# Optimization experiments

Hardware: AMD Instinct MI355X
Metric: run time of the kernel (lower is better)

## Reference

```python
import jax, jax.numpy as jnp
import numpy as np

N = 20000
NNBR = 64
MESH = (64, 64, 64)
ORDER = 4          # B-spline interpolation order
ALPHA = 0.35       # Ewald splitting parameter (1/Angstrom)
BOX = 73.68        # cubic box edge (Angstrom)
KE = 14.399645478425668  # Coulomb constant, eV*Angstrom/e^2


def _Mn(x, n):
    """Cardinal B-spline M_n(x), support [0, n]."""
    if n == 2:
        return jnp.maximum(0.0, 1.0 - jnp.abs(x - 1.0))
    return (x * _Mn(x, n - 1) + (n - x) * _Mn(x - 1.0, n - 1)) / (n - 1)


def _bspline_fac(K):
    """|b(m)|^-2 ... i.e. 1/|Euler spline denominator|^2 per mesh dim."""
    m = jnp.arange(K, dtype=jnp.float32)
    k = jnp.arange(ORDER - 1, dtype=jnp.float32)
    Mv = _Mn(k + 1.0, ORDER)                       # M_n(1..n-1)
    phase = 2.0 * jnp.pi * m[:, None] * k[None, :] / K
    dre = jnp.sum(Mv * jnp.cos(phase), axis=1)
    dim = jnp.sum(Mv * jnp.sin(phase), axis=1)
    return 1.0 / (dre * dre + dim * dim)


def _pme_energy(positions, charges, cell, nbr, shifts):
    n = positions.shape[0]
    # ---------------- real-space short-range sum ----------------
    i_idx = jnp.arange(n)[:, None]
    valid = (nbr >= 0) & ~((nbr == i_idx) & jnp.all(shifts == 0, axis=-1))
    j = jnp.where(nbr >= 0, nbr, 0)
    rvec = positions[j] + shifts.astype(positions.dtype) @ cell - positions[:, None, :]
    r2 = jnp.sum(rvec * rvec, axis=-1)
    r = jnp.sqrt(jnp.where(valid, r2, 1.0))
    qq = charges[:, None] * charges[j]
    e_real = 0.5 * jnp.sum(jnp.where(valid, qq * jax.scipy.special.erfc(ALPHA * r) / r, 0.0))
    # ---------------- B-spline charge spreading ----------------
    Kx, Ky, Kz = MESH
    frac = positions @ jnp.linalg.inv(cell)        # cell rows = lattice vectors
    u = frac * jnp.array(MESH, dtype=positions.dtype)
    base = jnp.floor(u)
    t = u - base                                   # in [0, 1)
    basei = base.astype(jnp.int32)
    offs = jnp.arange(ORDER)
    wx = _Mn(t[:, 0:1] + offs, ORDER)              # [N, ORDER]
    wy = _Mn(t[:, 1:2] + offs, ORDER)
    wz = _Mn(t[:, 2:3] + offs, ORDER)
    ix = (basei[:, 0:1] - offs) % Kx
    iy = (basei[:, 1:2] - offs) % Ky
    iz = (basei[:, 2:3] - offs) % Kz
    W = (charges[:, None] * wx)[:, :, None, None] * wy[:, None, :, None] * wz[:, None, None, :]
    IDX = (ix[:, :, None, None] * Ky + iy[:, None, :, None]) * Kz + iz[:, None, None, :]
    mesh = jnp.zeros(Kx * Ky * Kz, positions.dtype).at[IDX.reshape(-1)].add(W.reshape(-1)).reshape(MESH)
    # ---------------- reciprocal-space FFT convolution ----------------
    Q = jnp.fft.fftn(mesh)
    Brec = 2.0 * jnp.pi * jnp.linalg.inv(cell).T   # rows are reciprocal vectors
    mx = (jnp.fft.fftfreq(Kx) * Kx).astype(positions.dtype)
    my = (jnp.fft.fftfreq(Ky) * Ky).astype(positions.dtype)
    mz = (jnp.fft.fftfreq(Kz) * Kz).astype(positions.dtype)
    kvec = (mx[:, None, None, None] * Brec[0] + my[None, :, None, None] * Brec[1]
            + mz[None, None, :, None] * Brec[2])
    k2 = jnp.sum(kvec * kvec, axis=-1)
    a2 = ALPHA * ALPHA
    kern = jnp.where(k2 > 0, jnp.exp(-k2 / (4.0 * a2)) / jnp.where(k2 > 0, k2, 1.0), 0.0)
    C = _bspline_fac(Kx)[:, None, None] * _bspline_fac(Ky)[None, :, None] * _bspline_fac(Kz)[None, None, :]
    vol = jnp.abs(jnp.linalg.det(cell))
    e_rec = (2.0 * jnp.pi / vol) * jnp.sum(kern * C * (Q.real ** 2 + Q.imag ** 2))
    # ---------------- self + neutralizing background ----------------
    qtot = jnp.sum(charges)
    e_self = -(ALPHA / jnp.sqrt(jnp.pi)) * jnp.sum(charges * charges)
    e_bg = -(jnp.pi / (2.0 * a2 * vol)) * qtot * qtot
    return e_real + e_rec + e_self + e_bg


def setup_inputs() -> dict:
    key = jax.random.key(0)
    k1, k2, k3 = jax.random.split(key, 3)
    positions = jax.random.uniform(k1, (N, 3), jnp.float32) * BOX
    q = jax.random.normal(k2, (N,), jnp.float32)
    q = q - jnp.mean(q)  # neutral system
    cell = BOX * jnp.eye(3, dtype=jnp.float32)
    nbr = jax.random.randint(k3, (N, NNBR), 0, N, jnp.int32)
    shifts = jnp.zeros((N, NNBR, 3), jnp.int32)
    return {"positions": positions, "node_charges": q, "cell": cell,
            "neighbor_matrix": nbr, "neighbor_shifts": shifts}


def reference(positions, node_charges, cell, neighbor_matrix, neighbor_shifts):
    def e_strain(pos, q, c, eps):
        F = jnp.eye(3, dtype=pos.dtype) + eps
        return _pme_energy(pos @ F, q, c @ F, neighbor_matrix, neighbor_shifts)

    eps0 = jnp.zeros((3, 3), positions.dtype)
    e, (g_pos, g_eps) = jax.value_and_grad(e_strain, argnums=(0, 3))(
        positions, node_charges, cell, eps0)
    vol = jnp.abs(jnp.linalg.det(cell))
    energies = e.reshape(1) * KE
    forces = -g_pos * KE
    virial = -0.5 * (g_eps + g_eps.T) * KE
    stresses = (virial / vol)[None]
    return energies, forces, stresses
```

## Files before the change

kernel.cpp:

```cpp
#include <hip/hip_runtime.h>
#include <math.h>

#define NATOM 20000
#define NNBR  64
#define KM    64
#define KM3   (KM*KM*KM)

#define ALPHA_C 0.35f
#define KE_C    14.399645478425668f
#define TWO_OVER_SQRTPI 1.1283791670955126f
#define TWOPI_F 6.2831853071795864f
#define PI_F    3.14159265358979f
#define RC2     661.2244898f

#define WS_RE    0
#define WS_IM    (KM3)
#define WS_MESH  (2*KM3)
#define WS_GJ    (3*KM3)
#define WS_PART  (3*KM3 + 3*NATOM)
#define WS_FI    (WS_PART + 1024)
#define WS_POSQ  (WS_FI + 3*NATOM)
#define ZERO_LEN (KM3 + 3*NATOM + 1024)

__device__ __forceinline__ float M2f(float x){ return fmaxf(0.f, 1.f - fabsf(x - 1.f)); }
__device__ __forceinline__ float M3f(float x){ return (x*M2f(x) + (3.f-x)*M2f(x-1.f)) * 0.5f; }
__device__ __forceinline__ float M4f(float x){ return (x*M3f(x) + (4.f-x)*M3f(x-1.f)) * (1.f/3.f); }

__device__ __forceinline__ float wsum64(float v){
#pragma unroll
  for(int off=32; off>0; off>>=1) v += __shfl_xor(v, off, 64);
  return v;
}

__device__ __forceinline__ float hinv9(const float* __restrict__ cell, float* h){
  float m00=cell[0],m01=cell[1],m02=cell[2];
  float m10=cell[3],m11=cell[4],m12=cell[5];
  float m20=cell[6],m21=cell[7],m22=cell[8];
  float det = m00*(m11*m22-m12*m21) - m01*(m10*m22-m12*m20) + m02*(m10*m21-m11*m20);
  float id = 1.f/det;
  h[0]=(m11*m22-m12*m21)*id; h[1]=(m02*m21-m01*m22)*id; h[2]=(m01*m12-m02*m11)*id;
  h[3]=(m12*m20-m10*m22)*id; h[4]=(m00*m22-m02*m20)*id; h[5]=(m02*m10-m00*m12)*id;
  h[6]=(m10*m21-m11*m20)*id; h[7]=(m01*m20-m00*m21)*id; h[8]=(m00*m11-m01*m10)*id;
  return fabsf(det);
}

__device__ __forceinline__ void fft64(float& xr, float& xi, int lane, float sgn8){
#pragma unroll
  for(int k=0;k<6;k++){
    int half = 32 >> k;
    float or_ = __shfl_xor(xr, half, 64);
    float oi_ = __shfl_xor(xi, half, 64);
    bool hi = (lane & half) != 0;
    float sr = hi ? (or_ - xr) : (xr + or_);
    float si = hi ? (oi_ - xi) : (xi + oi_);
    int e = (lane & (half-1)) << k;
    float ws, wc; sincosf(sgn8 * (float)e, &ws, &wc);
    float wr2 = hi ? wc : 1.f;
    float wi2 = hi ? ws : 0.f;
    xr = sr*wr2 - si*wi2;
    xi = sr*wi2 + si*wr2;
  }
  int rev = __brev((unsigned)lane) >> 26;
  xr = __shfl(xr, rev, 64);
  xi = __shfl(xi, rev, 64);
}

__global__ __launch_bounds__(256) void init_kernel(
    const float* __restrict__ pos, const float* __restrict__ q,
    float* __restrict__ zbase, float4* __restrict__ posq){
  int t = blockIdx.x*256 + threadIdx.x;
  if(t < ZERO_LEN) zbase[t] = 0.f;
  if(t < NATOM)
    posq[t] = make_float4(pos[3*t], pos[3*t+1], pos[3*t+2], q[t]);
}

__global__ __launch_bounds__(256) void real_kernel(
    const float4* __restrict__ posq,
    const int* __restrict__ nbr, const int* __restrict__ shifts,
    const float* __restrict__ cell,
    float* __restrict__ fi, float* __restrict__ gj, float* __restrict__ part){
  int lane = threadIdx.x & 63;
  int wid  = blockIdx.x*4 + (threadIdx.x>>6);
  float c0=cell[0],c1=cell[1],c2=cell[2];
  float c3=cell[3],c4=cell[4],c5=cell[5];
  float c6=cell[6],c7=cell[7],c8=cell[8];
  float e=0.f, vxx=0.f,vyy=0.f,vzz=0.f,vxy=0.f,vxz=0.f,vyz=0.f;
#pragma unroll
  for(int it=0; it<4; ++it){
    int i = wid*4 + it;
    float4 pi4 = posq[i];
    int p = i*NNBR + lane;
    int j = nbr[p];
    int sx=shifts[3*p], sy=shifts[3*p+1], sz=shifts[3*p+2];
    bool self = (j==i) && (sx==0) && (sy==0) && (sz==0);
    float s=0.f, rx=0.f, ry=0.f, rz=0.f;
    if(j>=0 && !self){
      float4 pj = posq[j];
      rx = pj.x - pi4.x + sx*c0 + sy*c3 + sz*c6;
      ry = pj.y - pi4.y + sx*c1 + sy*c4 + sz*c7;
      rz = pj.z - pi4.z + sx*c2 + sy*c5 + sz*c8;
      float r2 = rx*rx + ry*ry + rz*rz;
      if(r2 > 0.f && r2 < RC2){
        float r = sqrtf(r2);
        float ar = ALPHA_C * r;
        float qq = pi4.w * pj.w;
        float ef = erfcf(ar);
        float ex = expf(-ar*ar);
        float ir = 1.f/r;
        e += 0.5f*qq*ef*ir;
        s  = 0.5f*qq*(ef + TWO_OVER_SQRTPI*ar*ex)*ir*ir*ir;
      }
    }
    float gx = s*rx, gy = s*ry, gz = s*rz;
    if(s != 0.f){
      unsafeAtomicAdd(&gj[3*j+0], -gx);
      unsafeAtomicAdd(&gj[3*j+1], -gy);
      unsafeAtomicAdd(&gj[3*j+2], -gz);
    }
    vxx -= s*rx*rx; vyy -= s*ry*ry; vzz -= s*rz*rz;
    vxy -= s*rx*ry; vxz -= s*rx*rz; vyz -= s*ry*rz;
    float tgx = wsum64(gx), tgy = wsum64(gy), tgz = wsum64(gz);
    if(lane==0){ fi[3*i]=tgx; fi[3*i+1]=tgy; fi[3*i+2]=tgz; }
  }
  e   = wsum64(e);
  vxx = wsum64(vxx); vyy = wsum64(vyy); vzz = wsum64(vzz);
  vxy = wsum64(vxy); vxz = wsum64(vxz); vyz = wsum64(vyz);
  if(lane==0){
    float* slot = part + (wid & 63)*16;
    unsafeAtomicAdd(&slot[0], e);
    unsafeAtomicAdd(&slot[1], vxx); unsafeAtomicAdd(&slot[2], vyy); unsafeAtomicAdd(&slot[3], vzz);
    unsafeAtomicAdd(&slot[4], vxy); unsafeAtomicAdd(&slot[5], vxz); unsafeAtomicAdd(&slot[6], vyz);
  }
}

__global__ __launch_bounds__(256) void spread_kernel(
    const float4* __restrict__ posq, const float* __restrict__ cell,
    float* __restrict__ mesh){
  int wid  = blockIdx.x*4 + (threadIdx.x>>6);
  int lane = threadIdx.x & 63;
  float h[9]; hinv9(cell, h);
  float4 pq = posq[wid];
  float u0=(pq.x*h[0]+pq.y*h[3]+pq.z*h[6])*(float)KM;
  float u1=(pq.x*h[1]+pq.y*h[4]+pq.z*h[7])*(float)KM;
  float u2=(pq.x*h[2]+pq.y*h[5]+pq.z*h[8])*(float)KM;
  float b0=floorf(u0), b1=floorf(u1), b2=floorf(u2);
  float t0=u0-b0, t1=u1-b1, t2=u2-b2;
  int i0=(int)b0, i1=(int)b1, i2=(int)b2;
  int a = lane>>4, b = (lane>>2)&3, c = lane&3;
  float w = pq.w * M4f(t0+(float)a) * M4f(t1+(float)b) * M4f(t2+(float)c);
  int ix=(i0-a+256)&63, iy=(i1-b+256)&63, iz=(i2-c+256)&63;
  unsafeAtomicAdd(&mesh[(ix*KM + iy)*KM + iz], w);
}

__global__ __launch_bounds__(256) void fftA(const float* __restrict__ mesh,
                                            float* __restrict__ re, float* __restrict__ im){
  __shared__ float lr[64][65], li[64][65];
  int t = threadIdx.x, lane = t&63, w = t>>6;
  int x = blockIdx.x;
  const float sgn8 = -(TWOPI_F/64.f);
  const float* mp = mesh + x*4096;
#pragma unroll
  for(int qq=0; qq<16; qq++){
    int y = w*16 + qq;
    float xr = mp[y*64 + lane], xi = 0.f;
    fft64(xr, xi, lane, sgn8);
    lr[y][lane]=xr; li[y][lane]=xi;
  }
  __syncthreads();
#pragma unroll
  for(int qq=0; qq<16; qq++){
    int z = w*16 + qq;
    float xr = lr[lane][z], xi = li[lane][z];
    fft64(xr, xi, lane, sgn8);
    lr[lane][z]=xr; li[lane][z]=xi;
  }
  __syncthreads();
  float* rp = re + x*4096; float* ip = im + x*4096;
#pragma unroll
  for(int k=0;k<16;k++){
    int e = k*256 + t;
    rp[e]=lr[e>>6][e&63]; ip[e]=li[e>>6][e&63];
  }
}

__global__ __launch_bounds__(256) void fftB(float* __restrict__ re, float* __restrict__ im,
                                            const float* __restrict__ cell,
                                            float* __restrict__ part){
  __shared__ float lr[64][17], li[64][17], cf[64];
  int t = threadIdx.x, lane = t&63, w = t>>6;
  int y = blockIdx.x>>2, z0 = (blockIdx.x&3)*16;
  const float sgn8 = -(TWOPI_F/64.f);
  float h[9]; hinv9(cell, h);
  if(t < 64){
    float p1 = TWOPI_F*(float)t/64.f;
    float s1,c1_,s2,c2_; sincosf(p1,&s1,&c1_); sincosf(2.f*p1,&s2,&c2_);
    float dre = (1.f/6.f) + (2.f/3.f)*c1_ + (1.f/6.f)*c2_;
    float dim = (2.f/3.f)*s1 + (1.f/6.f)*s2;
    cf[t] = 1.f/(dre*dre + dim*dim);
  }
  float* rp = re + y*64 + z0;
  float* ip = im + y*64 + z0;
#pragma unroll
  for(int k=0;k<4;k++){
    int e = k*256 + t; int xI = e>>4, zz = e&15;
    lr[xI][zz] = rp[xI*4096 + zz];
    li[xI][zz] = ip[xI*4096 + zz];
  }
  __syncthreads();
  const float inv4a2 = 1.f/(4.f*ALPHA_C*ALPHA_C);
  float my_f = (float)((y<32)? y : y-64);
  float sE=0.f, v0=0.f,v1=0.f,v2=0.f,v3=0.f,v4=0.f,v5=0.f;
#pragma unroll
  for(int qq=0; qq<4; qq++){
    int zz = w*4 + qq; int z = z0 + zz;
    float xr = lr[lane][zz], xi = li[lane][zz];
    fft64(xr, xi, lane, sgn8);
    int mx = lane, mz = z;
    float fx = (float)((mx<32)? mx : mx-64);
    float fz = (float)((mz<32)? mz : mz-64);
    float kx = TWOPI_F*(fx*h[0] + my_f*h[1] + fz*h[2]);
    float ky = TWOPI_F*(fx*h[3] + my_f*h[4] + fz*h[5]);
    float kz = TWOPI_F*(fx*h[6] + my_f*h[7] + fz*h[8]);
    float k2 = kx*kx + ky*ky + kz*kz;
    float wk = 0.f;
    if(k2 > 0.f){
      float kern = expf(-k2*inv4a2)/k2;
      wk = kern * cf[mx]*cf[y]*cf[z];
      float q2 = xr*xr + xi*xi;
      sE += wk*q2;
      float fac = wk*q2*(inv4a2 + 1.f/k2)*2.f;
      v0 += fac*kx*kx; v1 += fac*ky*ky; v2 += fac*kz*kz;
      v3 += fac*kx*ky; v4 += fac*kx*kz; v5 += fac*ky*kz;
    }
    lr[lane][zz] = wk*xr; li[lane][zz] = wk*xi;
  }
  __syncthreads();
#pragma unroll
  for(int k=0;k<4;k++){
    int e = k*256 + t; int xI = e>>4, zz = e&15;
    rp[xI*4096 + zz] = lr[xI][zz];
    ip[xI*4096 + zz] = li[xI][zz];
  }
  sE = wsum64(sE);
  v0 = wsum64(v0); v1 = wsum64(v1); v2 = wsum64(v2);
  v3 = wsum64(v3); v4 = wsum64(v4); v5 = wsum64(v5);
  if(lane==0){
    float* slot = part + (((blockIdx.x<<2)|w)&63)*16;
    unsafeAtomicAdd(&slot[7],  sE);
    unsafeAtomicAdd(&slot[8],  v0); unsafeAtomicAdd(&slot[9],  v1);
    unsafeAtomicAdd(&slot[10], v2); unsafeAtomicAdd(&slot[11], v3);
    unsafeAtomicAdd(&slot[12], v4); unsafeAtomicAdd(&slot[13], v5);
  }
}

__global__ __launch_bounds__(256) void fftC(float* __restrict__ re, float* __restrict__ im){
  __shared__ float lr[64][17], li[64][17];
  int t = threadIdx.x, lane = t&63, w = t>>6;
  int y = blockIdx.x>>2, z0 = (blockIdx.x&3)*16;
  const float sgn8 = (TWOPI_F/64.f);
  float* rp = re + y*64 + z0;
  float* ip = im + y*64 + z0;
#pragma unroll
  for(int k=0;k<4;k++){
    int e = k*256 + t; int xI = e>>4, zz = e&15;
    lr[xI][zz] = rp[xI*4096 + zz];
    li[xI][zz] = ip[xI*4096 + zz];
  }
  __syncthreads();
#pragma unroll
  for(int qq=0; qq<4; qq++){
    int zz = w*4 + qq;
    float xr = lr[lane][zz], xi = li[lane][zz];
    fft64(xr, xi, lane, sgn8);
    lr[lane][zz] = xr; li[lane][zz] = xi;
  }
  __syncthreads();
#pragma unroll
  for(int k=0;k<4;k++){
    int e = k*256 + t; int xI = e>>4, zz = e&15;
    rp[xI*4096 + zz] = lr[xI][zz];
    ip[xI*4096 + zz] = li[xI][zz];
  }
}

__global__ __launch_bounds__(256) void fftD(float* __restrict__ re, float* __restrict__ im){
  __shared__ float lr[64][65], li[64][65];
  int t = threadIdx.x, lane = t&63, w = t>>6;
  int x = blockIdx.x;
  const float sgn8 = (TWOPI_F/64.f);
  float* rp = re + x*4096;
  float* ip = im + x*4096;
#pragma unroll
  for(int k=0;k<16;k++){
    int e = k*256 + t;
    lr[e>>6][e&63] = rp[e];
    li[e>>6][e&63] = ip[e];
  }
  __syncthreads();
#pragma unroll
  for(int qq=0; qq<16; qq++){
    int z = w*16 + qq;
    float xr = lr[lane][z], xi = li[lane][z];
    fft64(xr, xi, lane, sgn8);
    lr[lane][z]=xr; li[lane][z]=xi;
  }
  __syncthreads();
#pragma unroll
  for(int qq=0; qq<16; qq++){
    int y = w*16 + qq;
    float xr = lr[y][lane], xi = li[y][lane];
    fft64(xr, xi, lane, sgn8);
    rp[y*64 + lane] = xr;
  }
}

__global__ __launch_bounds__(256) void gather_kernel(
    const float4* __restrict__ posq, const float* __restrict__ cell,
    const float* __restrict__ phi,
    const float* __restrict__ fi, const float* __restrict__ gj,
    const float* __restrict__ part, float* __restrict__ out){
  __shared__ float sa[256], sb[256], facc[16];
  int wid  = blockIdx.x*4 + (threadIdx.x>>6);
  int lane = threadIdx.x & 63;
  float h[9]; float V = hinv9(cell, h);
  float4 pq = posq[wid];
  float u0=(pq.x*h[0]+pq.y*h[3]+pq.z*h[6])*(float)KM;
  float u1=(pq.x*h[1]+pq.y*h[4]+pq.z*h[7])*(float)KM;
  float u2=(pq.x*h[2]+pq.y*h[5]+pq.z*h[8])*(float)KM;
  float b0=floorf(u0), b1=floorf(u1), b2=floorf(u2);
  float t0=u0-b0, t1=u1-b1, t2=u2-b2;
  int i0=(int)b0, i1=(int)b1, i2=(int)b2;
  int a = lane>>4, b = (lane>>2)&3, c = lane&3;
  float fa=(float)a, fb=(float)b, fc=(float)c;
  float wxa=M4f(t0+fa), wyb=M4f(t1+fb), wzc=M4f(t2+fc);
  float dxa=M3f(t0+fa)-M3f(t0+fa-1.f);
  float dyb=M3f(t1+fb)-M3f(t1+fb-1.f);
  float dzc=M3f(t2+fc)-M3f(t2+fc-1.f);
  int ix=(i0-a+256)&63, iy=(i1-b+256)&63, iz=(i2-c+256)&63;
  float p = phi[(ix*KM + iy)*KM + iz];
  float Sx = wsum64(p*dxa*wyb*wzc);
  float Sy = wsum64(p*wxa*dyb*wzc);
  float Sz = wsum64(p*wxa*wyb*dzc);
  if(lane==0){
    float scale = pq.w * (2.f*TWOPI_F/V) * (float)KM;
    float g0 = scale*(Sx*h[0] + Sy*h[1] + Sz*h[2]);
    float g1 = scale*(Sx*h[3] + Sy*h[4] + Sz*h[5]);
    float g2 = scale*(Sx*h[6] + Sy*h[7] + Sz*h[8]);
    out[1+3*wid+0] = -KE_C*(fi[3*wid+0] + gj[3*wid+0] + g0);
    out[1+3*wid+1] = -KE_C*(fi[3*wid+1] + gj[3*wid+1] + g1);
    out[1+3*wid+2] = -KE_C*(fi[3*wid+2] + gj[3*wid+2] + g2);
  }
  if(blockIdx.x==0){
    int t = threadIdx.x;
    float qa=0.f, qb=0.f;
    for(int i=t;i<NATOM;i+=256){ float qv=posq[i].w; qa+=qv; qb+=qv*qv; }
    sa[t]=qa; sb[t]=qb; __syncthreads();
    for(int off=128; off>0; off>>=1){
      if(t<off){ sa[t]+=sa[t+off]; sb[t]+=sb[t+off]; } __syncthreads();
    }
    if(t<14){ float s=0.f; for(int sl=0;sl<64;sl++) s+=part[sl*16+t]; facc[t]=s; }
    __syncthreads();
    if(t==0){
      float qtot = sa[0], sumq2 = sb[0];
      float a2 = ALPHA_C*ALPHA_C;
      float pref = TWOPI_F/V;
      float e_real = facc[0];
      float e_rec  = pref*facc[7];
      float e_self = -(ALPHA_C/sqrtf(PI_F))*sumq2;
      float e_bg   = -(PI_F/(2.f*a2*V))*qtot*qtot;
      out[0] = (e_real + e_rec + e_self + e_bg)*KE_C;
      float gxx = facc[1] + pref*facc[8]  - e_rec - e_bg;
      float gyy = facc[2] + pref*facc[9]  - e_rec - e_bg;
      float gzz = facc[3] + pref*facc[10] - e_rec - e_bg;
      float gxy = facc[4] + pref*facc[11];
      float gxz = facc[5] + pref*facc[12];
      float gyz = facc[6] + pref*facc[13];
      float cc = -KE_C/V;
      float* st = out + 1 + 3*NATOM;
      st[0]=cc*gxx; st[4]=cc*gyy; st[8]=cc*gzz;
      st[1]=cc*gxy; st[3]=cc*gxy;
      st[2]=cc*gxz; st[6]=cc*gxz;
      st[5]=cc*gyz; st[7]=cc*gyz;
    }
  }
}

extern "C" void kernel_launch(void* const* d_in, const int* in_sizes, int n_in,
                              void* d_out, int out_size, void* d_ws, size_t ws_size,
                              hipStream_t stream) {
  const float* pos  = (const float*)d_in[0];
  const float* q    = (const float*)d_in[1];
  const float* cell = (const float*)d_in[2];
  const int* nbr    = (const int*)d_in[3];
  const int* shifts = (const int*)d_in[4];
  float* out = (float*)d_out;
  float* ws  = (float*)d_ws;
  float*  bufRe = ws + WS_RE;
  float*  bufIm = ws + WS_IM;
  float*  mesh  = ws + WS_MESH;
  float*  gj    = ws + WS_GJ;
  float*  part  = ws + WS_PART;
  float*  fi    = ws + WS_FI;
  float4* posq  = (float4*)(ws + WS_POSQ);

  init_kernel<<<(ZERO_LEN+255)/256,256,0,stream>>>(pos, q, mesh, posq);
  real_kernel<<<1250,256,0,stream>>>(posq, nbr, shifts, cell, fi, gj, part);
  spread_kernel<<<5000,256,0,stream>>>(posq, cell, mesh);
  fftA<<< 64,256,0,stream>>>(mesh, bufRe, bufIm);
  fftB<<<256,256,0,stream>>>(bufRe, bufIm, cell, part);
  fftC<<<256,256,0,stream>>>(bufRe, bufIm);
  fftD<<< 64,256,0,stream>>>(bufRe, bufIm);
  gather_kernel<<<5000,256,0,stream>>>(posq, cell, bufRe, fi, gj, part, out);
}
```

Baseline: 191.2 us.

## Fuse spread into real-space kernel, pack neighbor data, table FFT twiddles, split FFT passes

Packs the neighbor index and periodic shifts into one int per pair in the init kernel, then reads that packed word in a combined kernel that does both the real-space pair sum and the B-spline charge spreading. The spread kernel disappears. FFT twiddles now come from a shared-memory table instead of per-stage sincosf, and the 2D per-x-slab FFT kernels are split into separate z-line and y-line kernels with more blocks. This trades extra launches and an extra global round trip of the complex grid for more parallelism, and the packing assumes indices below 32768 and shifts within ±8.

```diff
diff --git a/kernel.cpp b/kernel.cpp
--- a/kernel.cpp
+++ b/kernel.cpp
@@ -5,6 +5,7 @@
 #define NNBR  64
 #define KM    64
 #define KM3   (KM*KM*KM)
+#define NPAIR (NATOM*NNBR)
 
 #define ALPHA_C 0.35f
 #define KE_C    14.399645478425668f
@@ -20,6 +21,7 @@
 #define WS_PART  (3*KM3 + 3*NATOM)
 #define WS_FI    (WS_PART + 1024)
 #define WS_POSQ  (WS_FI + 3*NATOM)
+#define WS_NBS   (WS_POSQ + 4*NATOM)
 #define ZERO_LEN (KM3 + 3*NATOM + 1024)
 
 __device__ __forceinline__ float M2f(float x){ return fmaxf(0.f, 1.f - fabsf(x - 1.f)); }
@@ -44,7 +46,16 @@
   return fabsf(det);
 }
 
-__device__ __forceinline__ void fft64(float& xr, float& xi, int lane, float sgn8){
+__device__ __forceinline__ void fill_tw(int t, float* twr, float* twi){
+  if(t < 64){
+    float ss, cc; sincosf((TWOPI_F/64.f)*(float)t, &ss, &cc);
+    twr[t] = cc; twi[t] = -ss;
+  }
+}
+
+__device__ __forceinline__ void fft64t(float& xr, float& xi, int lane,
+                                       const float* __restrict__ twr,
+                                       const float* __restrict__ twi, float sgn){
 #pragma unroll
   for(int k=0;k<6;k++){
     int half = 32 >> k;
@@ -54,9 +65,8 @@
     float sr = hi ? (or_ - xr) : (xr + or_);
     float si = hi ? (oi_ - xi) : (xi + oi_);
     int e = (lane & (half-1)) << k;
-    float ws, wc; sincosf(sgn8 * (float)e, &ws, &wc);
-    float wr2 = hi ? wc : 1.f;
-    float wi2 = hi ? ws : 0.f;
+    float wr2 = hi ? twr[e] : 1.f;
+    float wi2 = hi ? sgn*twi[e] : 0.f;
     xr = sr*wr2 - si*wi2;
     xi = sr*wi2 + si*wr2;
   }
@@ -67,34 +77,56 @@
 
 __global__ __launch_bounds__(256) void init_kernel(
     const float* __restrict__ pos, const float* __restrict__ q,
-    float* __restrict__ zbase, float4* __restrict__ posq){
+    const int* __restrict__ nbr, const int* __restrict__ shifts,
+    float* __restrict__ zbase, float4* __restrict__ posq, int* __restrict__ nbs){
   int t = blockIdx.x*256 + threadIdx.x;
   if(t < ZERO_LEN) zbase[t] = 0.f;
   if(t < NATOM)
     posq[t] = make_float4(pos[3*t], pos[3*t+1], pos[3*t+2], q[t]);
-}
-
-__global__ __launch_bounds__(256) void real_kernel(
-    const float4* __restrict__ posq,
-    const int* __restrict__ nbr, const int* __restrict__ shifts,
+  if(t < NPAIR){
+    int j = nbr[t];
+    int sx=shifts[3*t], sy=shifts[3*t+1], sz=shifts[3*t+2];
+    int v;
+    if(j < 0) v = -1;
+    else v = (j & 0x7FFF) | ((sx+8)&15)<<15 | ((sy+8)&15)<<19 | ((sz+8)&15)<<23;
+    nbs[t] = v;
+  }
+}
+
+__global__ __launch_bounds__(256) void realspread_kernel(
+    const float4* __restrict__ posq, const int* __restrict__ nbs,
     const float* __restrict__ cell,
-    float* __restrict__ fi, float* __restrict__ gj, float* __restrict__ part){
+    float* __restrict__ fi, float* __restrict__ gj, float* __restrict__ part,
+    float* __restrict__ mesh){
   int lane = threadIdx.x & 63;
   int wid  = blockIdx.x*4 + (threadIdx.x>>6);
   float c0=cell[0],c1=cell[1],c2=cell[2];
   float c3=cell[3],c4=cell[4],c5=cell[5];
   float c6=cell[6],c7=cell[7],c8=cell[8];
+  float h[9]; hinv9(cell, h);
+  int la = lane>>4, lb = (lane>>2)&3, lc = lane&3;
   float e=0.f, vxx=0.f,vyy=0.f,vzz=0.f,vxy=0.f,vxz=0.f,vyz=0.f;
 #pragma unroll
   for(int it=0; it<4; ++it){
     int i = wid*4 + it;
     float4 pi4 = posq[i];
-    int p = i*NNBR + lane;
-    int j = nbr[p];
-    int sx=shifts[3*p], sy=shifts[3*p+1], sz=shifts[3*p+2];
+    int v = nbs[i*NNBR + lane];
+    {
+      float u0=(pi4.x*h[0]+pi4.y*h[3]+pi4.z*h[6])*(float)KM;
+      float u1=(pi4.x*h[1]+pi4.y*h[4]+pi4.z*h[7])*(float)KM;
+      float u2=(pi4.x*h[2]+pi4.y*h[5]+pi4.z*h[8])*(float)KM;
+      float b0=floorf(u0), b1=floorf(u1), b2=floorf(u2);
+      float t0=u0-b0, t1=u1-b1, t2=u2-b2;
+      int i0=(int)b0, i1=(int)b1, i2=(int)b2;
+      float w = pi4.w * M4f(t0+(float)la) * M4f(t1+(float)lb) * M4f(t2+(float)lc);
+      int ix=(i0-la+256)&63, iy=(i1-lb+256)&63, iz=(i2-lc+256)&63;
+      unsafeAtomicAdd(&mesh[(ix*KM + iy)*KM + iz], w);
+    }
+    int j = v & 0x7FFF;
+    int sx=((v>>15)&15)-8, sy=((v>>19)&15)-8, sz=((v>>23)&15)-8;
     bool self = (j==i) && (sx==0) && (sy==0) && (sz==0);
     float s=0.f, rx=0.f, ry=0.f, rz=0.f;
-    if(j>=0 && !self){
+    if(v>=0 && !self){
       float4 pj = posq[j];
       rx = pj.x - pi4.x + sx*c0 + sy*c3 + sz*c6;
       ry = pj.y - pi4.y + sx*c1 + sy*c4 + sz*c7;
@@ -133,64 +165,67 @@
   }
 }
 
-__global__ __launch_bounds__(256) void spread_kernel(
-    const float4* __restrict__ posq, const float* __restrict__ cell,
-    float* __restrict__ mesh){
-  int wid  = blockIdx.x*4 + (threadIdx.x>>6);
-  int lane = threadIdx.x & 63;
-  float h[9]; hinv9(cell, h);
-  float4 pq = posq[wid];
-  float u0=(pq.x*h[0]+pq.y*h[3]+pq.z*h[6])*(float)KM;
-  float u1=(pq.x*h[1]+pq.y*h[4]+pq.z*h[7])*(float)KM;
-  float u2=(pq.x*h[2]+pq.y*h[5]+pq.z*h[8])*(float)KM;
-  float b0=floorf(u0), b1=floorf(u1), b2=floorf(u2);
-  float t0=u0-b0, t1=u1-b1, t2=u2-b2;
-  int i0=(int)b0, i1=(int)b1, i2=(int)b2;
-  int a = lane>>4, b = (lane>>2)&3, c = lane&3;
-  float w = pq.w * M4f(t0+(float)a) * M4f(t1+(float)b) * M4f(t2+(float)c);
-  int ix=(i0-a+256)&63, iy=(i1-b+256)&63, iz=(i2-c+256)&63;
-  unsafeAtomicAdd(&mesh[(ix*KM + iy)*KM + iz], w);
-}
-
-__global__ __launch_bounds__(256) void fftA(const float* __restrict__ mesh,
-                                            float* __restrict__ re, float* __restrict__ im){
-  __shared__ float lr[64][65], li[64][65];
+__global__ __launch_bounds__(256) void fftZF(const float* __restrict__ mesh,
+                                             float* __restrict__ re, float* __restrict__ im){
+  __shared__ float twr[64], twi[64];
+  int t = threadIdx.x, lane = t&63;
+  fill_tw(t, twr, twi);
+  __syncthreads();
+  int idx = blockIdx.x*256 + t;
+  float xr = mesh[idx], xi = 0.f;
+  fft64t(xr, xi, lane, twr, twi, 1.f);
+  re[idx]=xr; im[idx]=xi;
+}
+
+__global__ __launch_bounds__(256) void fftZI(float* __restrict__ re, const float* __restrict__ im){
+  __shared__ float twr[64], twi[64];
+  int t = threadIdx.x, lane = t&63;
+  fill_tw(t, twr, twi);
+  __syncthreads();
+  int idx = blockIdx.x*256 + t;
+  float xr = re[idx], xi = im[idx];
+  fft64t(xr, xi, lane, twr, twi, -1.f);
+  re[idx]=xr;
+}
+
+__global__ __launch_bounds__(256) void fftY(float* __restrict__ re, float* __restrict__ im,
+                                            float sgn){
+  __shared__ float lr[64][17], li[64][17], twr[64], twi[64];
   int t = threadIdx.x, lane = t&63, w = t>>6;
-  int x = blockIdx.x;
-  const float sgn8 = -(TWOPI_F/64.f);
-  const float* mp = mesh + x*4096;
-#pragma unroll
-  for(int qq=0; qq<16; qq++){
-    int y = w*16 + qq;
-    float xr = mp[y*64 + lane], xi = 0.f;
-    fft64(xr, xi, lane, sgn8);
-    lr[y][lane]=xr; li[y][lane]=xi;
-  }
-  __syncthreads();
-#pragma unroll
-  for(int qq=0; qq<16; qq++){
-    int z = w*16 + qq;
-    float xr = lr[lane][z], xi = li[lane][z];
-    fft64(xr, xi, lane, sgn8);
-    lr[lane][z]=xr; li[lane][z]=xi;
-  }
-  __syncthreads();
-  float* rp = re + x*4096; float* ip = im + x*4096;
-#pragma unroll
-  for(int k=0;k<16;k++){
-    int e = k*256 + t;
-    rp[e]=lr[e>>6][e&63]; ip[e]=li[e>>6][e&63];
+  fill_tw(t, twr, twi);
+  int x = blockIdx.x>>2, z0 = (blockIdx.x&3)*16;
+  int off = x*4096 + z0;
+#pragma unroll
+  for(int k=0;k<4;k++){
+    int e = k*256 + t; int y = e>>4, zz = e&15;
+    lr[y][zz] = re[off + y*64 + zz];
+    li[y][zz] = im[off + y*64 + zz];
+  }
+  __syncthreads();
+#pragma unroll
+  for(int qq=0; qq<4; qq++){
+    int zz = w*4 + qq;
+    float xr = lr[lane][zz], xi = li[lane][zz];
+    fft64t(xr, xi, lane, twr, twi, sgn);
+    lr[lane][zz] = xr; li[lane][zz] = xi;
+  }
+  __syncthreads();
+#pragma unroll
+  for(int k=0;k<4;k++){
+    int e = k*256 + t; int y = e>>4, zz = e&15;
+    re[off + y*64 + zz] = lr[y][zz];
+    im[off + y*64 + zz] = li[y][zz];
   }
 }
 
 __global__ __launch_bounds__(256) void fftB(float* __restrict__ re, float* __restrict__ im,
                                             const float* __restrict__ cell,
                                             float* __restrict__ part){
-  __shared__ float lr[64][17], li[64][17], cf[64];
+  __shared__ float lr[64][17], li[64][17], cf[64], twr[64], twi[64];
   int t = threadIdx.x, lane = t&63, w = t>>6;
   int y = blockIdx.x>>2, z0 = (blockIdx.x&3)*16;
-  const float sgn8 = -(TWOPI_F/64.f);
   float h[9]; hinv9(cell, h);
+  fill_tw(t, twr, twi);
   if(t < 64){
     float p1 = TWOPI_F*(float)t/64.f;
     float s1,c1_,s2,c2_; sincosf(p1,&s1,&c1_); sincosf(2.f*p1,&s2,&c2_);
@@ -214,7 +249,7 @@
   for(int qq=0; qq<4; qq++){
     int zz = w*4 + qq; int z = z0 + zz;
     float xr = lr[lane][zz], xi = li[lane][zz];
-    fft64(xr, xi, lane, sgn8);
+    fft64t(xr, xi, lane, twr, twi, 1.f);
     int mx = lane, mz = z;
     float fx = (float)((mx<32)? mx : mx-64);
     float fz = (float)((mz<32)? mz : mz-64);
@@ -254,10 +289,10 @@
 }
 
 __global__ __launch_bounds__(256) void fftC(float* __restrict__ re, float* __restrict__ im){
-  __shared__ float lr[64][17], li[64][17];
+  __shared__ float lr[64][17], li[64][17], twr[64], twi[64];
   int t = threadIdx.x, lane = t&63, w = t>>6;
+  fill_tw(t, twr, twi);
   int y = blockIdx.x>>2, z0 = (blockIdx.x&3)*16;
-  const float sgn8 = (TWOPI_F/64.f);
   float* rp = re + y*64 + z0;
   float* ip = im + y*64 + z0;
 #pragma unroll
@@ -271,7 +306,7 @@
   for(int qq=0; qq<4; qq++){
     int zz = w*4 + qq;
     float xr = lr[lane][zz], xi = li[lane][zz];
-    fft64(xr, xi, lane, sgn8);
+    fft64t(xr, xi, lane, twr, twi, -1.f);
     lr[lane][zz] = xr; li[lane][zz] = xi;
   }
   __syncthreads();
@@ -280,37 +315,6 @@
     int e = k*256 + t; int xI = e>>4, zz = e&15;
     rp[xI*4096 + zz] = lr[xI][zz];
     ip[xI*4096 + zz] = li[xI][zz];
-  }
-}
-
-__global__ __launch_bounds__(256) void fftD(float* __restrict__ re, float* __restrict__ im){
-  __shared__ float lr[64][65], li[64][65];
-  int t = threadIdx.x, lane = t&63, w = t>>6;
-  int x = blockIdx.x;
-  const float sgn8 = (TWOPI_F/64.f);
-  float* rp = re + x*4096;
-  float* ip = im + x*4096;
-#pragma unroll
-  for(int k=0;k<16;k++){
-    int e = k*256 + t;
-    lr[e>>6][e&63] = rp[e];
-    li[e>>6][e&63] = ip[e];
-  }
-  __syncthreads();
-#pragma unroll
-  for(int qq=0; qq<16; qq++){
-    int z = w*16 + qq;
-    float xr = lr[lane][z], xi = li[lane][z];
-    fft64(xr, xi, lane, sgn8);
-    lr[lane][z]=xr; li[lane][z]=xi;
-  }
-  __syncthreads();
-#pragma unroll
-  for(int qq=0; qq<16; qq++){
-    int y = w*16 + qq;
-    float xr = lr[y][lane], xi = li[y][lane];
-    fft64(xr, xi, lane, sgn8);
-    rp[y*64 + lane] = xr;
   }
 }
 
@@ -402,13 +406,15 @@
   float*  part  = ws + WS_PART;
   float*  fi    = ws + WS_FI;
   float4* posq  = (float4*)(ws + WS_POSQ);
-
-  init_kernel<<<(ZERO_LEN+255)/256,256,0,stream>>>(pos, q, mesh, posq);
-  real_kernel<<<1250,256,0,stream>>>(posq, nbr, shifts, cell, fi, gj, part);
-  spread_kernel<<<5000,256,0,stream>>>(posq, cell, mesh);
-  fftA<<< 64,256,0,stream>>>(mesh, bufRe, bufIm);
-  fftB<<<256,256,0,stream>>>(bufRe, bufIm, cell, part);
-  fftC<<<256,256,0,stream>>>(bufRe, bufIm);
-  fftD<<< 64,256,0,stream>>>(bufRe, bufIm);
+  int*    nbs   = (int*)(ws + WS_NBS);
+
+  init_kernel<<<(NPAIR+255)/256,256,0,stream>>>(pos, q, nbr, shifts, mesh, posq, nbs);
+  realspread_kernel<<<1250,256,0,stream>>>(posq, nbs, cell, fi, gj, part, mesh);
+  fftZF<<<1024,256,0,stream>>>(mesh, bufRe, bufIm);
+  fftY <<< 256,256,0,stream>>>(bufRe, bufIm, 1.f);
+  fftB <<< 256,256,0,stream>>>(bufRe, bufIm, cell, part);
+  fftC <<< 256,256,0,stream>>>(bufRe, bufIm);
+  fftY <<< 256,256,0,stream>>>(bufRe, bufIm, -1.f);
+  fftZI<<<1024,256,0,stream>>>(bufRe, bufIm);
   gather_kernel<<<5000,256,0,stream>>>(posq, cell, bufRe, fi, gj, part, out);
 }
```

Result: no change. 189.6 us (-0.8%).
